# Kernel optimization log

Hardware: AMD Instinct MI355X
Metric: run time of the kernel (lower is better)

Reference implementation:

```python
import jax, jax.numpy as jnp
import numpy as np

B, T, D, H = 64, 512, 300, 256
K1, K2 = 10, 12


def lstm(x, mask, W, b):
    # x: [B,T,Din], mask: [B,T] bool. TF LSTMCell gate order i,j,f,o; forget_bias=1.0.
    xT = jnp.swapaxes(x, 0, 1)  # [T,B,Din]
    mT = jnp.swapaxes(mask, 0, 1)  # [T,B]
    Hd = b.shape[0] // 4
    Bn = x.shape[0]

    def step(carry, inp):
        h, c = carry
        xt, mt = inp
        z = jnp.concatenate([xt, h], axis=-1) @ W + b
        i, j, f, o = jnp.split(z, 4, axis=-1)
        c_new = jax.nn.sigmoid(f + 1.0) * c + jax.nn.sigmoid(i) * jnp.tanh(j)
        h_new = jax.nn.sigmoid(o) * jnp.tanh(c_new)
        m = mt[:, None]
        c2 = jnp.where(m, c_new, c)
        h2 = jnp.where(m, h_new, h)
        out = jnp.where(m, h_new, jnp.zeros_like(h_new))  # dynamic_rnn zeros past length
        return (h2, c2), out

    init = (jnp.zeros((Bn, Hd), x.dtype), jnp.zeros((Bn, Hd), x.dtype))
    _, outs = jax.lax.scan(step, init, (xT, mT))
    return jnp.swapaxes(outs, 0, 1)  # [B,T,H]


def reverse_seq(x, lengths):
    # reverse each sequence along time up to its length (padding stays in place)
    t = jnp.arange(x.shape[1])
    idx = lengths[:, None] - 1 - t[None, :]
    idx = jnp.where(idx >= 0, idx, t[None, :])
    return jnp.take_along_axis(x, idx[:, :, None], axis=1)


def bilstm(x, lengths, mask, Wf, bf, Wb, bb):
    fw = lstm(x, mask, Wf, bf)
    xr = reverse_seq(x, lengths)
    bw = reverse_seq(lstm(xr, mask, Wb, bb), lengths)
    return jnp.concatenate([fw, bw], axis=-1)  # [B,T,2H]


def crf_nll(logits, labels, lengths, trans):
    # negative crf_log_likelihood per example
    Tn = logits.shape[1]
    t = jnp.arange(Tn)
    mask = t[None, :] < lengths[:, None]  # [B,T]
    unary = jnp.take_along_axis(logits, labels[:, :, None], 2)[:, :, 0]
    unary_score = jnp.sum(jnp.where(mask, unary, 0.0), axis=1)
    tr = trans[labels[:, :-1], labels[:, 1:]]
    trans_score = jnp.sum(jnp.where(mask[:, 1:], tr, 0.0), axis=1)

    def step(alpha, inp):
        lt, mt = inp  # [B,K], [B]
        new = jax.nn.logsumexp(alpha[:, :, None] + trans[None, :, :], axis=1) + lt
        return jnp.where(mt[:, None], new, alpha), None

    alpha, _ = jax.lax.scan(
        step, logits[:, 0],
        (jnp.swapaxes(logits[:, 1:], 0, 1), jnp.swapaxes(mask[:, 1:], 0, 1)))
    logZ = jax.nn.logsumexp(alpha, axis=-1)
    return logZ - (unary_score + trans_score)


def setup_inputs() -> dict:
    key = jax.random.key(0)
    ks = jax.random.split(key, 24)
    s = 0.05
    inp = {
        'embedded_words': jax.random.normal(ks[0], (B, T, D), jnp.float32),
        'sentence_lenghts': jax.random.randint(ks[1], (B,), 1, T + 1, jnp.int32),
        'labels': jax.random.randint(ks[2], (B, T), 0, K1, jnp.int32),
    }
    i = 3
    for scope in ('t1', 't2', 'sh'):
        for d in ('fw', 'bw'):
            inp[f'{scope}_{d}_W'] = jax.random.normal(ks[i], (D + H, 4 * H), jnp.float32) * s
            inp[f'{scope}_{d}_b'] = jnp.zeros((4 * H,), jnp.float32)
            i += 1
    inp['W1'] = jax.random.normal(ks[i], (4 * H, K1), jnp.float32) * s; i += 1
    inp['b1'] = jnp.zeros((K1,), jnp.float32)
    inp['W2'] = jax.random.normal(ks[i], (4 * H, K2), jnp.float32) * s; i += 1
    inp['b2'] = jnp.zeros((K2,), jnp.float32)
    inp['trans1'] = jax.random.normal(ks[i], (K1, K1), jnp.float32) * s; i += 1
    inp['trans2'] = jax.random.normal(ks[i], (K2, K2), jnp.float32) * s
    return inp


def reference(embedded_words, sentence_lenghts, labels,
              t1_fw_W, t1_fw_b, t1_bw_W, t1_bw_b,
              t2_fw_W, t2_fw_b, t2_bw_W, t2_bw_b,
              sh_fw_W, sh_fw_b, sh_bw_W, sh_bw_b,
              W1, b1, W2, b2, trans1, trans2):
    mask = jnp.arange(embedded_words.shape[1])[None, :] < sentence_lenghts[:, None]
    t1 = bilstm(embedded_words, sentence_lenghts, mask, t1_fw_W, t1_fw_b, t1_bw_W, t1_bw_b)
    t2 = bilstm(embedded_words, sentence_lenghts, mask, t2_fw_W, t2_fw_b, t2_bw_W, t2_bw_b)
    sh = bilstm(embedded_words, sentence_lenghts, mask, sh_fw_W, sh_fw_b, sh_bw_W, sh_bw_b)
    logits1 = jnp.concatenate([t1, sh], axis=-1) @ W1 + b1  # [B,T,K1]
    logits2 = jnp.concatenate([t2, sh], axis=-1) @ W2 + b2  # [B,T,K2]
    nll1 = crf_nll(logits1, labels, sentence_lenghts, trans1)
    nll2 = crf_nll(logits2, labels, sentence_lenghts, trans2)
    return jnp.stack([nll1, nll2])  # [2,B]
```

## Files before the change

### kernel.cpp

```cpp
#include <hip/hip_runtime.h>
#include <cstdint>
#include <cstddef>

#define B_ 64
#define T_ 512
#define D_ 300
#define DP_ 320
#define H_ 256
#define G4_ 1024
#define NL_ 6

typedef float f32x4 __attribute__((ext_vector_type(4)));
typedef __bf16 bf16x8 __attribute__((ext_vector_type(8)));

struct WPtrs { const float* W[NL_]; const float* Bv[NL_]; };

__device__ __forceinline__ unsigned short f2bf(float f){
  unsigned int u = __float_as_uint(f);
  unsigned int r = u + 0x7FFFu + ((u >> 16) & 1u);
  return (unsigned short)(r >> 16);
}
__device__ __forceinline__ float bf2f(unsigned int s){
  return __uint_as_float((s & 0xFFFFu) << 16);
}
__device__ __forceinline__ float fast_sig(float x){
  return __builtin_amdgcn_rcpf(1.f + __builtin_amdgcn_exp2f(-1.4426950408889634f * x));
}
__device__ __forceinline__ float fast_tanh(float x){
  return 1.f - 2.f * __builtin_amdgcn_rcpf(1.f + __builtin_amdgcn_exp2f(2.8853900817779268f * x));
}
__device__ __forceinline__ void store8bf(unsigned short* p, const unsigned short v[8]){
  uint4 u;
  u.x = (unsigned)v[0] | ((unsigned)v[1] << 16);
  u.y = (unsigned)v[2] | ((unsigned)v[3] << 16);
  u.z = (unsigned)v[4] | ((unsigned)v[5] << 16);
  u.w = (unsigned)v[6] | ((unsigned)v[7] << 16);
  *(uint4*)p = u;
}

__global__ void k_prep_x(const float* __restrict__ x, const int* __restrict__ len,
                         unsigned short* __restrict__ xf){
  int idx = blockIdx.x * 256 + threadIdx.x;
  int lane = idx & 63;
  int kt = (idx >> 6) % 10;
  int r1 = idx / 640;
  int bt = r1 & 3;
  int r2 = r1 >> 2;
  int t = r2 & 511;
  int dir = r2 >> 9;
  if (dir >= 2) return;
  int bb = bt * 16 + (lane & 15);
  int k0 = kt * 32 + (lane >> 4) * 8;
  int L = len[bb];
  int tsrc = dir ? ((t < L) ? (L - 1 - t) : t) : t;
  const float* xs = x + ((size_t)bb * T_ + tsrc) * D_;
  unsigned short v[8];
  #pragma unroll
  for (int e = 0; e < 8; e++){
    int k = k0 + e;
    v[e] = f2bf(k < D_ ? xs[k] : 0.f);
  }
  store8bf(xf + ((size_t)idx) * 8, v);
}

__global__ void k_prep_w(WPtrs wp, unsigned short* __restrict__ whp,
                         unsigned short* __restrict__ wxp,
                         const float* __restrict__ W1, const float* __restrict__ W2,
                         float* __restrict__ w1t, float* __restrict__ w2t){
  int idx = blockIdx.x * 256 + threadIdx.x;
  const int nWh = NL_ * 16 * 4 * 8 * 64;
  const int nWx = NL_ * 16 * 10 * 4 * 64;
  if (idx < nWh){
    int lane = idx & 63, kt = (idx >> 6) & 7, g = (idx >> 9) & 3, s = (idx >> 11) & 15, l = idx >> 15;
    int col = g * 256 + s * 16 + (lane & 15);
    int k0 = kt * 32 + (lane >> 4) * 8;
    const float* W = wp.W[l];
    unsigned short v[8];
    #pragma unroll
    for (int e = 0; e < 8; e++) v[e] = f2bf(W[(size_t)(D_ + k0 + e) * G4_ + col]);
    store8bf(whp + ((((size_t)(l * 16 + s) * 4 + g) * 8 + kt) * 64 + lane) * 8, v);
  } else if (idx < nWh + nWx){
    int i2 = idx - nWh;
    int lane = i2 & 63;
    int g = (i2 >> 6) & 3;
    int r = i2 >> 8;
    int kt = r % 10;
    int r2 = r / 10;
    int s = r2 & 15, l = r2 >> 4;
    int col = g * 256 + s * 16 + (lane & 15);
    int k0 = kt * 32 + (lane >> 4) * 8;
    const float* W = wp.W[l];
    unsigned short v[8];
    #pragma unroll
    for (int e = 0; e < 8; e++){
      int k = k0 + e;
      v[e] = f2bf(k < D_ ? W[(size_t)k * G4_ + col] : 0.f);
    }
    store8bf(wxp + ((((size_t)(l * 16 + s) * 10 + kt) * 4 + g) * 64 + lane) * 8, v);
  } else if (idx < nWh + nWx + 16384){
    int i2 = idx - nWh - nWx;
    int h = i2 & 1023, k = i2 >> 10;
    w1t[k * G4_ + h] = (k < 10) ? W1[h * 10 + k] : 0.f;
  } else if (idx < nWh + nWx + 32768){
    int i2 = idx - nWh - nWx - 16384;
    int h = i2 & 1023, k = i2 >> 10;
    w2t[k * G4_ + h] = (k < 12) ? W2[h * 12 + k] : 0.f;
  }
}

#define LOADH() \
  { _Pragma("unroll") \
    for (int kt = 0; kt < 8; kt++) \
      _Pragma("unroll") \
      for (int jj = 0; jj < 4; jj++) \
        hq[kt][jj] = __hip_atomic_load(hreg + (kt * 4 + jj) * 64 + lane, \
                                       __ATOMIC_RELAXED, __HIP_MEMORY_SCOPE_AGENT); \
  }

#define UNPACKH() \
  { accor = 0u; \
    _Pragma("unroll") \
    for (int kt = 0; kt < 8; kt++){ \
      union { unsigned u[4]; bf16x8 v; } uu; \
      _Pragma("unroll") \
      for (int jj = 0; jj < 4; jj++){ \
        unsigned lo = (unsigned)hq[kt][jj]; \
        unsigned hi = (unsigned)(hq[kt][jj] >> 32); \
        uu.u[jj] = __builtin_amdgcn_perm(hi, lo, 0x05040100u); \
        accor |= __builtin_amdgcn_perm(hi, lo, 0x07060302u) ^ cmpw; \
      } \
      Ah[kt] = uu.v; \
    } }

#define HMFMA() \
  { _Pragma("unroll") \
    for (int g = 0; g < 4; g++) acc[g] = accX[g]; \
    _Pragma("unroll") \
    for (int kt = 0; kt < 8; kt++) \
      _Pragma("unroll") \
      for (int g = 0; g < 4; g++) \
        acc[g] = __builtin_amdgcn_mfma_f32_16x16x32_bf16(Ah[kt], Bh[g][kt], acc[g], 0, 0, 0); \
  }

__global__ __launch_bounds__(256, 1) void k_rec(
    const unsigned short* __restrict__ whp, const unsigned short* __restrict__ wxp,
    const unsigned short* __restrict__ xf, WPtrs wp, const int* __restrict__ len,
    unsigned long long* __restrict__ hpub, unsigned short* __restrict__ ho){
  int l = blockIdx.x >> 4;
  int s = blockIdx.x & 15;
  int tid = threadIdx.x, lane = tid & 63, w = tid >> 6;
  const int dir = l & 1;

  __shared__ unsigned int lds_pub[1024];

  bf16x8 Bh[4][8];
  #pragma unroll
  for (int g = 0; g < 4; g++)
    #pragma unroll
    for (int kt = 0; kt < 8; kt++)
      Bh[g][kt] = *(const bf16x8*)(whp + ((((size_t)(l * 16 + s) * 4 + g) * 8 + kt) * 64 + lane) * 8);
  bf16x8 Bx[10][4];
  #pragma unroll
  for (int kt = 0; kt < 10; kt++)
    #pragma unroll
    for (int g = 0; g < 4; g++)
      Bx[kt][g] = *(const bf16x8*)(wxp + ((((size_t)(l * 16 + s) * 10 + kt) * 4 + g) * 64 + lane) * 8);

  float bias[4];
  #pragma unroll
  for (int g = 0; g < 4; g++) bias[g] = wp.Bv[l][g * 256 + s * 16 + (lane & 15)];

  float c4[4] = {0.f, 0.f, 0.f, 0.f};
  float h4[4] = {0.f, 0.f, 0.f, 0.f};
  int Lr[4];
  #pragma unroll
  for (int r = 0; r < 4; r++) Lr[r] = len[w * 16 + (lane >> 4) * 4 + r];

  int unit = s * 16 + (lane & 15);
  const int kt_s = s >> 1, qc0 = (s & 1) * 2;
  const int rp = lane & 15, g2 = lane >> 4;
  const int pjj = (rp >> 1) & 3, pqh = rp >> 3, ppp = rp & 1;
  const int lbase = w * 256 + (pjj * 2 + pqh) * 32 + ppp;
  unsigned long long* lds64 = (unsigned long long*)lds_pub;
  const int rb0 = w * 128 + ((lane >> 4) * 2 + 0) * 16 + (lane & 15);
  const int rb1 = rb0 + 16;
  const size_t so0 = (size_t)(kt_s * 4 + (lane >> 4)) * 64 + qc0 * 16 + (lane & 15);

  for (int t = 0; t < T_; t++){
    f32x4 accX[4];
    #pragma unroll
    for (int g = 0; g < 4; g++){ accX[g].x = 0.f; accX[g].y = 0.f; accX[g].z = 0.f; accX[g].w = 0.f; }
    const unsigned short* xt = xf + (((size_t)(dir * T_ + t) * 4 + w) * 10) * 512;
    #pragma unroll
    for (int kt = 0; kt < 10; kt++){
      bf16x8 Ax = *(const bf16x8*)(xt + (size_t)kt * 512 + lane * 8);
      #pragma unroll
      for (int g = 0; g < 4; g++)
        accX[g] = __builtin_amdgcn_mfma_f32_16x16x32_bf16(Ax, Bx[kt][g], accX[g], 0, 0, 0);
    }
    f32x4 acc[4];
    if (t > 0){
      const unsigned long long* hreg = hpub + (((size_t)(l * 2 + ((t - 1) & 1)) * 4 + w) * 2048);
      unsigned long long hq[8][4];
      bf16x8 Ah[8];
      unsigned accor;
      const unsigned cmpw = ((unsigned)(t - 1)) * 0x00010001u;
      LOADH();
      UNPACKH();
      HMFMA();
      bool stale = __any(accor != 0);
      int tries = 0;
      while (stale && tries < 8192){
        tries++;
        __builtin_amdgcn_s_sleep(1);
        LOADH();
        UNPACKH();
        stale = __any(accor != 0);
        if (!stale){ HMFMA(); }
      }
    } else {
      #pragma unroll
      for (int g = 0; g < 4; g++) acc[g] = accX[g];
    }
    unsigned short hpb[4], hov[4];
    #pragma unroll
    for (int r = 0; r < 4; r++){
      float gi = acc[0][r] + bias[0], gj = acc[1][r] + bias[1];
      float gf = acc[2][r] + bias[2], go = acc[3][r] + bias[3];
      float cn = fast_sig(gf + 1.f) * c4[r] + fast_sig(gi) * fast_tanh(gj);
      float hn = fast_sig(go) * fast_tanh(cn);
      bool m = (t < Lr[r]);
      c4[r] = m ? cn : c4[r];
      h4[r] = m ? hn : h4[r];
      hpb[r] = f2bf(h4[r]);
      hov[r] = f2bf(m ? hn : 0.f);
    }
    unsigned tagt = ((unsigned)t) << 16;
    #pragma unroll
    for (int rr = 0; rr < 4; rr++)
      lds_pub[lbase + (g2 * 4 + rr) * 2] = tagt | (unsigned)hpb[rr];
    unsigned long long* hrego = hpub + (((size_t)(l * 2 + (t & 1)) * 4 + w) * 2048);
    __hip_atomic_store(hrego + so0,      lds64[rb0], __ATOMIC_RELAXED, __HIP_MEMORY_SCOPE_AGENT);
    __hip_atomic_store(hrego + so0 + 16, lds64[rb1], __ATOMIC_RELAXED, __HIP_MEMORY_SCOPE_AGENT);
    #pragma unroll
    for (int rr = 0; rr < 4; rr++){
      int b = w * 16 + (lane >> 4) * 4 + rr;
      int tdst = dir ? ((t < Lr[rr]) ? (Lr[rr] - 1 - t) : t) : t;
      ho[(((size_t)l * B_ + b) * T_ + tdst) * H_ + unit] = hov[rr];
    }
  }
}

__global__ void k_logits(const unsigned short* __restrict__ ho,
                         const float* __restrict__ w1t, const float* __restrict__ w2t,
                         const float* __restrict__ b1, const float* __restrict__ b2,
                         float* __restrict__ lgt){
  int gid = blockIdx.x * 4 + (threadIdx.x >> 6);
  int lane = threadIdx.x & 63;
  int b = gid >> 9, t = gid & 511;
  float hv[6][4];
  #pragma unroll
  for (int lgi = 0; lgi < 6; lgi++){
    const unsigned short* hrow = ho + (((size_t)lgi * B_ + b) * T_ + t) * H_;
    uint2 u = *(const uint2*)(hrow + lane * 4);
    hv[lgi][0] = bf2f(u.x); hv[lgi][1] = bf2f(u.x >> 16);
    hv[lgi][2] = bf2f(u.y); hv[lgi][3] = bf2f(u.y >> 16);
  }
  float s1[10], s2[12];
  #pragma unroll
  for (int k = 0; k < 10; k++) s1[k] = 0.f;
  #pragma unroll
  for (int k = 0; k < 12; k++) s2[k] = 0.f;
  const int seg1[4] = {0, 1, 4, 5};
  const int seg2[4] = {2, 3, 4, 5};
  #pragma unroll
  for (int k = 0; k < 10; k++){
    #pragma unroll
    for (int ii = 0; ii < 4; ii++){
      float4 wv = *(const float4*)(w1t + k * G4_ + ii * 256 + lane * 4);
      int lgi = seg1[ii];
      s1[k] += hv[lgi][0] * wv.x + hv[lgi][1] * wv.y + hv[lgi][2] * wv.z + hv[lgi][3] * wv.w;
    }
  }
  #pragma unroll
  for (int k = 0; k < 12; k++){
    #pragma unroll
    for (int ii = 0; ii < 4; ii++){
      float4 wv = *(const float4*)(w2t + k * G4_ + ii * 256 + lane * 4);
      int lgi = seg2[ii];
      s2[k] += hv[lgi][0] * wv.x + hv[lgi][1] * wv.y + hv[lgi][2] * wv.z + hv[lgi][3] * wv.w;
    }
  }
  #pragma unroll
  for (int k = 0; k < 10; k++)
    #pragma unroll
    for (int d = 1; d < 64; d <<= 1) s1[k] += __shfl_xor(s1[k], d, 64);
  #pragma unroll
  for (int k = 0; k < 12; k++)
    #pragma unroll
    for (int d = 1; d < 64; d <<= 1) s2[k] += __shfl_xor(s2[k], d, 64);
  if (lane == 0){
    float* o1 = lgt + ((size_t)(0 * B_ + b) * T_ + t) * 16;
    float* o2 = lgt + ((size_t)(1 * B_ + b) * T_ + t) * 16;
    #pragma unroll
    for (int k = 0; k < 10; k++) o1[k] = s1[k] + b1[k];
    #pragma unroll
    for (int k = 0; k < 12; k++) o2[k] = s2[k] + b2[k];
  }
}

__global__ void k_crf(const float* __restrict__ lgt, const int* __restrict__ labels,
                      const int* __restrict__ len, const float* __restrict__ trans1,
                      const float* __restrict__ trans2, float* __restrict__ out){
  int gid = blockIdx.x * 4 + (threadIdx.x >> 6);
  int lane = threadIdx.x & 63;
  int tau = gid >> 6;
  int b = gid & 63;
  int K = tau ? 12 : 10;
  const float* tr = tau ? trans2 : trans1;
  const float* lgp = lgt + (size_t)(tau * B_ + b) * T_ * 16;
  int L = len[b];
  int k2 = lane & 15;
  const float LOG2E = 1.4426950408889634f;
  const float LN2 = 0.6931471805599453f;
  float Et[12];
  #pragma unroll
  for (int k1 = 0; k1 < 12; k1++)
    Et[k1] = (k1 < K && k2 < K) ? __builtin_amdgcn_exp2f(LOG2E * tr[k1 * K + k2]) : 0.f;
  float alpha = (k2 < K) ? lgp[k2] : -1e30f;
  for (int t = 1; t < L; t++){
    float m = alpha;
    #pragma unroll
    for (int d = 1; d < 16; d <<= 1) m = fmaxf(m, __shfl_xor(m, d, 16));
    float e = __builtin_amdgcn_exp2f(LOG2E * (alpha - m));
    float ss = 0.f;
    #pragma unroll
    for (int k1 = 0; k1 < 12; k1++)
      ss += __shfl(e, k1, 16) * Et[k1];
    float na = m + LN2 * __builtin_amdgcn_logf(ss) + lgp[t * 16 + k2];
    alpha = (k2 < K) ? na : -1e30f;
  }
  float m2 = alpha;
  #pragma unroll
  for (int d = 1; d < 16; d <<= 1) m2 = fmaxf(m2, __shfl_xor(m2, d, 16));
  float e2 = __builtin_amdgcn_exp2f(LOG2E * (alpha - m2));
  #pragma unroll
  for (int d = 1; d < 16; d <<= 1) e2 += __shfl_xor(e2, d, 16);
  float logZ = m2 + LN2 * __builtin_amdgcn_logf(e2);
  float us = 0.f;
  const int* lab = labels + b * T_;
  for (int t0 = lane; t0 < L; t0 += 64){
    int la = lab[t0];
    us += lgp[t0 * 16 + la];
    if (t0 >= 1) us += tr[lab[t0 - 1] * K + la];
  }
  #pragma unroll
  for (int d = 1; d < 64; d <<= 1) us += __shfl_xor(us, d, 64);
  if (lane == 0) out[tau * B_ + b] = logZ - us;
}

extern "C" void kernel_launch(void* const* d_in, const int* in_sizes, int n_in,
                              void* d_out, int out_size, void* d_ws, size_t ws_size,
                              hipStream_t stream){
  const float* x = (const float*)d_in[0];
  const int* len = (const int*)d_in[1];
  const int* labels = (const int*)d_in[2];
  WPtrs wp;
  for (int l = 0; l < NL_; l++){
    wp.W[l] = (const float*)d_in[3 + 2 * l];
    wp.Bv[l] = (const float*)d_in[4 + 2 * l];
  }
  const float* W1 = (const float*)d_in[15];
  const float* b1 = (const float*)d_in[16];
  const float* W2 = (const float*)d_in[17];
  const float* b2 = (const float*)d_in[18];
  const float* trans1 = (const float*)d_in[19];
  const float* trans2 = (const float*)d_in[20];

  char* ws = (char*)d_ws;
  const size_t SZ_HPUB = (size_t)NL_ * 2 * 4 * 2048 * 8;
  const size_t O_WHP = SZ_HPUB;
  const size_t SZ_WHP = (size_t)NL_ * H_ * G4_ * 2;
  const size_t O_WXP = O_WHP + SZ_WHP;
  const size_t SZ_WXP = (size_t)NL_ * DP_ * G4_ * 2;
  const size_t O_XF  = O_WXP + SZ_WXP;
  const size_t SZ_XF = 2ull * T_ * 4 * 10 * 64 * 8 * 2;
  const size_t O_HO  = O_XF + SZ_XF;
  const size_t SZ_HO = (size_t)NL_ * B_ * T_ * H_ * 2;
  const size_t O_LGT = O_HO + SZ_HO;
  const size_t SZ_LGT = 2ull * B_ * T_ * 16 * 4;
  const size_t O_W1T = O_LGT + SZ_LGT;
  const size_t O_W2T = O_W1T + 65536;

  unsigned long long* hpub = (unsigned long long*)(ws + 0);
  unsigned short* whp = (unsigned short*)(ws + O_WHP);
  unsigned short* wxp = (unsigned short*)(ws + O_WXP);
  unsigned short* xf  = (unsigned short*)(ws + O_XF);
  unsigned short* ho  = (unsigned short*)(ws + O_HO);
  float* lgt = (float*)(ws + O_LGT);
  float* w1t = (float*)(ws + O_W1T);
  float* w2t = (float*)(ws + O_W2T);

  hipMemsetAsync(hpub, 0xFF, SZ_HPUB, stream);
  k_prep_x<<<10240, 256, 0, stream>>>(x, len, xf);
  k_prep_w<<<1856, 256, 0, stream>>>(wp, whp, wxp, W1, W2, w1t, w2t);
  k_rec<<<96, 256, 0, stream>>>(whp, wxp, xf, wp, len, hpub, ho);
  k_logits<<<8192, 256, 0, stream>>>(ho, w1t, w2t, b1, b2, lgt);
  k_crf<<<32, 256, 0, stream>>>(lgt, labels, len, trans1, trans2, (float*)d_out);
}
```

Baseline: 2.622 ms.

## Pin each LSTM layer's blocks to one XCD and poll h via sc0 loads

The recurrent kernel now launches 256 blocks. Each block reads its XCC id and claims a slot from a per-XCC counter, so the 16 blocks of one layer all run on the same XCD and extra blocks exit. Polling for the previous hidden state now uses inline global_load_dwordx2 with sc0 instead of agent-scope atomic loads, and publishing uses plain stores. This is meant to keep the cross-block hidden-state exchange inside one XCD's L2 and cut per-step sync latency. The MFMA is moved after the stale-check loop. This relies on at least 16 blocks landing on each of XCDs 0-5 and on sc0 coherence within an XCD, which risks a deadlock or stale reads if placement differs.

```diff
diff --git a/kernel.cpp b/kernel.cpp
--- a/kernel.cpp
+++ b/kernel.cpp
@@ -108,13 +108,19 @@
   }
 }
 
-#define LOADH() \
+#define LOADH_SC0() \
   { _Pragma("unroll") \
-    for (int kt = 0; kt < 8; kt++) \
+    for (int g2i = 0; g2i < 4; g2i++){ \
+      const unsigned long long* bp = hbase + (size_t)g2i * 512; \
       _Pragma("unroll") \
-      for (int jj = 0; jj < 4; jj++) \
-        hq[kt][jj] = __hip_atomic_load(hreg + (kt * 4 + jj) * 64 + lane, \
-                                       __ATOMIC_RELAXED, __HIP_MEMORY_SCOPE_AGENT); \
+      for (int j2 = 0; j2 < 8; j2++){ \
+        asm volatile("global_load_dwordx2 %0, %1, off offset:%2 sc0" \
+                     : "=v"(hq[g2i * 2 + (j2 >> 2)][j2 & 3]) \
+                     : "v"(bp), "i"(j2 * 512)); \
+      } \
+    } \
+    asm volatile("s_waitcnt vmcnt(0)" ::: "memory"); \
+    __builtin_amdgcn_sched_barrier(0); \
   }
 
 #define UNPACKH() \
@@ -132,22 +138,22 @@
       Ah[kt] = uu.v; \
     } }
 
-#define HMFMA() \
-  { _Pragma("unroll") \
-    for (int g = 0; g < 4; g++) acc[g] = accX[g]; \
-    _Pragma("unroll") \
-    for (int kt = 0; kt < 8; kt++) \
-      _Pragma("unroll") \
-      for (int g = 0; g < 4; g++) \
-        acc[g] = __builtin_amdgcn_mfma_f32_16x16x32_bf16(Ah[kt], Bh[g][kt], acc[g], 0, 0, 0); \
-  }
-
 __global__ __launch_bounds__(256, 1) void k_rec(
     const unsigned short* __restrict__ whp, const unsigned short* __restrict__ wxp,
     const unsigned short* __restrict__ xf, WPtrs wp, const int* __restrict__ len,
-    unsigned long long* __restrict__ hpub, unsigned short* __restrict__ ho){
-  int l = blockIdx.x >> 4;
-  int s = blockIdx.x & 15;
+    unsigned long long* __restrict__ hpub, unsigned short* __restrict__ ho,
+    int* __restrict__ pool){
+  __shared__ int role_sh;
+  int xcc;
+  asm volatile("s_getreg_b32 %0, hwreg(HW_REG_XCC_ID)" : "=s"(xcc));
+  if (threadIdx.x == 0){
+    int r = atomicAdd(&pool[xcc & 7], 1);
+    role_sh = (xcc < NL_ && r < 16) ? r : -1;
+  }
+  __syncthreads();
+  int s = role_sh;
+  if (s < 0) return;
+  int l = xcc;
   int tid = threadIdx.x, lane = tid & 63, w = tid >> 6;
   const int dir = l & 1;
 
@@ -200,24 +206,27 @@
     }
     f32x4 acc[4];
     if (t > 0){
-      const unsigned long long* hreg = hpub + (((size_t)(l * 2 + ((t - 1) & 1)) * 4 + w) * 2048);
+      const unsigned long long* hbase =
+          hpub + (((size_t)(l * 2 + ((t - 1) & 1)) * 4 + w) * 2048) + lane;
       unsigned long long hq[8][4];
       bf16x8 Ah[8];
       unsigned accor;
       const unsigned cmpw = ((unsigned)(t - 1)) * 0x00010001u;
-      LOADH();
+      LOADH_SC0();
       UNPACKH();
-      HMFMA();
-      bool stale = __any(accor != 0);
       int tries = 0;
-      while (stale && tries < 8192){
-        tries++;
+      while (__any(accor != 0) && ++tries < 4096){
         __builtin_amdgcn_s_sleep(1);
-        LOADH();
+        LOADH_SC0();
         UNPACKH();
-        stale = __any(accor != 0);
-        if (!stale){ HMFMA(); }
       }
+      #pragma unroll
+      for (int g = 0; g < 4; g++) acc[g] = accX[g];
+      #pragma unroll
+      for (int kt = 0; kt < 8; kt++)
+        #pragma unroll
+        for (int g = 0; g < 4; g++)
+          acc[g] = __builtin_amdgcn_mfma_f32_16x16x32_bf16(Ah[kt], Bh[g][kt], acc[g], 0, 0, 0);
     } else {
       #pragma unroll
       for (int g = 0; g < 4; g++) acc[g] = accX[g];
@@ -240,8 +249,8 @@
     for (int rr = 0; rr < 4; rr++)
       lds_pub[lbase + (g2 * 4 + rr) * 2] = tagt | (unsigned)hpb[rr];
     unsigned long long* hrego = hpub + (((size_t)(l * 2 + (t & 1)) * 4 + w) * 2048);
-    __hip_atomic_store(hrego + so0,      lds64[rb0], __ATOMIC_RELAXED, __HIP_MEMORY_SCOPE_AGENT);
-    __hip_atomic_store(hrego + so0 + 16, lds64[rb1], __ATOMIC_RELAXED, __HIP_MEMORY_SCOPE_AGENT);
+    hrego[so0]      = lds64[rb0];
+    hrego[so0 + 16] = lds64[rb1];
     #pragma unroll
     for (int rr = 0; rr < 4; rr++){
       int b = w * 16 + (lane >> 4) * 4 + rr;
@@ -391,6 +400,7 @@
   const size_t SZ_LGT = 2ull * B_ * T_ * 16 * 4;
   const size_t O_W1T = O_LGT + SZ_LGT;
   const size_t O_W2T = O_W1T + 65536;
+  const size_t O_POOL = O_W2T + 65536;
 
   unsigned long long* hpub = (unsigned long long*)(ws + 0);
   unsigned short* whp = (unsigned short*)(ws + O_WHP);
@@ -400,11 +410,13 @@
   float* lgt = (float*)(ws + O_LGT);
   float* w1t = (float*)(ws + O_W1T);
   float* w2t = (float*)(ws + O_W2T);
+  int* pool = (int*)(ws + O_POOL);
 
   hipMemsetAsync(hpub, 0xFF, SZ_HPUB, stream);
+  hipMemsetAsync(pool, 0, 64, stream);
   k_prep_x<<<10240, 256, 0, stream>>>(x, len, xf);
   k_prep_w<<<1856, 256, 0, stream>>>(wp, whp, wxp, W1, W2, w1t, w2t);
-  k_rec<<<96, 256, 0, stream>>>(whp, wxp, xf, wp, len, hpub, ho);
+  k_rec<<<256, 256, 0, stream>>>(whp, wxp, xf, wp, len, hpub, ho, pool);
   k_logits<<<8192, 256, 0, stream>>>(ho, w1t, w2t, b1, b2, lgt);
   k_crf<<<32, 256, 0, stream>>>(lgt, labels, len, trans1, trans2, (float*)d_out);
 }
```

Measured after the change: 2.719 ms. 1.04x slower.
